# Kernel optimization log

Hardware: AMD Instinct MI355X
Metric: run time of the kernel (lower is better)

## Reference

```python
import jax, jax.numpy as jnp
import numpy as np

B, C, O, N, T, K = 4, 64, 64, 32768, 4, 9
PAD, DIL = 4, 1  # padding*dilation, dilation
SIGMA = 0.05
EPS_BN = 1e-5


def _gather_ch(x, idx):
    # x: [B, C, N], idx: [B, N] -> gather along last dim per channel
    idx3 = jnp.broadcast_to(idx[:, None, :], x.shape)
    return jnp.take_along_axis(x, idx3, axis=-1)


def _weighted_conv(x, coords, w):
    # x: [B,C,N], coords: [B,3,N], w: [O,C,K]
    xp = jnp.pad(x, ((0, 0), (0, 0), (PAD, PAD)))
    cp = jnp.pad(coords, ((0, 0), (0, 0), (PAD, PAD)))
    win_idx = jnp.arange(N)[:, None] + jnp.arange(K) * DIL  # [N, K]
    win = xp[:, :, win_idx]   # [B,C,N,K]
    cwin = cp[:, :, win_idx]  # [B,3,N,K]
    d = cwin - cwin[:, :, :, K // 2:K // 2 + 1]
    s = jnp.sum(d * d, axis=1)                    # [B,N,K]
    r = jnp.sqrt(jnp.where(s > 0, s, 1.0))
    r = jnp.where(s > 0, r, 0.0)
    wgt = jnp.maximum(1.0 - r / SIGMA, 0.0)       # [B,N,K]
    return jnp.einsum('bcnk,bnk,ock->bon', win, wgt, w)


def _bn(x, g, b):
    # training-mode BatchNorm1d over (B, N)
    m = jnp.mean(x, axis=(0, 2), keepdims=True)
    v = jnp.var(x, axis=(0, 2), keepdims=True)
    return g[None, :, None] * (x - m) * jax.lax.rsqrt(v + EPS_BN) + b[None, :, None]


def setup_inputs() -> dict:
    key = jax.random.key(0)
    ks = jax.random.split(key, 12)
    inp = jax.random.normal(ks[0], (B, C, N), dtype=jnp.float32)
    # coords in a small box so sigma=0.05 yields non-trivial weights
    multi_coords = jax.random.uniform(ks[1], (B, 3, N, T), dtype=jnp.float32) * 0.02
    indices = jax.random.randint(ks[2], (B, N, T), 0, N, dtype=jnp.int32)
    reindices = jax.random.randint(ks[3], (B, N, T), 0, N, dtype=jnp.int32)
    fan = C * K
    conv_w = jax.random.normal(ks[4], (T, O, C, K), dtype=jnp.float32) / np.sqrt(fan)
    bn_gamma = jnp.ones((T, O), dtype=jnp.float32)
    bn_beta = jnp.zeros((T, O), dtype=jnp.float32)
    fusion_w = jax.random.normal(ks[5], (O, T * O), dtype=jnp.float32) / np.sqrt(T * O)
    fusion_b = jnp.zeros((O,), dtype=jnp.float32)
    fusion_gamma = jnp.ones((O,), dtype=jnp.float32)
    fusion_beta = jnp.zeros((O,), dtype=jnp.float32)
    return {"input": inp, "multi_coords": multi_coords, "indices": indices,
            "reindices": reindices, "conv_w": conv_w, "bn_gamma": bn_gamma,
            "bn_beta": bn_beta, "fusion_w": fusion_w, "fusion_b": fusion_b,
            "fusion_gamma": fusion_gamma, "fusion_beta": fusion_beta}


def reference(input, multi_coords, indices, reindices, conv_w, bn_gamma, bn_beta,
              fusion_w, fusion_b, fusion_gamma, fusion_beta):
    outs = []
    for i in range(T):  # fixed small set of 4 Hilbert orders
        x = _gather_ch(input, indices[:, :, i])            # [B,C,N]
        x = _weighted_conv(x, multi_coords[:, :, :, i], conv_w[i])  # [B,O,N]
        x = _bn(x, bn_gamma[i], bn_beta[i])
        x = _gather_ch(x, reindices[:, :, i])
        outs.append(x)
    cat = jnp.concatenate(outs, axis=1)                    # [B, T*O, N]
    y = jnp.einsum('bcn,oc->bon', cat, fusion_w) + fusion_b[None, :, None]
    y = _bn(y, fusion_gamma, fusion_beta)
    return jax.nn.relu(y)
```

## Files before the change

kernel.cpp:

```cpp
#include <hip/hip_runtime.h>
#include <hip/hip_bf16.h>

#define BB 4
#define CC 64
#define OO 64
#define NN 32768
#define TT 4
#define KK 9
#define PADW 4
#define SIGMA 0.05f
#define EPS_BN 1e-5f

typedef __attribute__((ext_vector_type(8))) short bf16x8;
typedef __attribute__((ext_vector_type(4))) float f32x4;

__device__ __forceinline__ unsigned short f2bf(float f) {
  __hip_bfloat16 h = __float2bfloat16(f);
  return *reinterpret_cast<unsigned short*>(&h);
}
__device__ __forceinline__ unsigned int pkbf(float a, float b) {
  float2 t; t.x = a; t.y = b;
  __hip_bfloat162 h = __float22bfloat162_rn(t);
  unsigned int r;
  __builtin_memcpy(&r, &h, 4);
  return r;
}

__global__ __launch_bounds__(256) void transpose_kernel(
    const float* __restrict__ inp, unsigned short* __restrict__ xTb)
{
  const int n0 = blockIdx.x * 64;
  const int b  = blockIdx.y;
  const int tid = threadIdx.x;
  __shared__ float xt[64][65];
  {
    int nl = tid & 63, c4 = tid >> 6;
    #pragma unroll
    for (int i = 0; i < 16; ++i) {
      int c = c4 * 16 + i;
      xt[c][nl] = inp[((size_t)(b*CC + c))*NN + n0 + nl];
    }
  }
  __syncthreads();
  {
    int nl = tid >> 2, cq = tid & 3;
    unsigned int pk[8];
    #pragma unroll
    for (int i = 0; i < 8; ++i) {
      int c = cq*16 + i*2;
      pk[i] = pkbf(xt[c][nl], xt[c+1][nl]);
    }
    unsigned int* dst = (unsigned int*)(xTb + (((size_t)b*NN) + n0 + nl)*CC + cq*16);
    ((int4*)dst)[0] = make_int4((int)pk[0],(int)pk[1],(int)pk[2],(int)pk[3]);
    ((int4*)dst)[1] = make_int4((int)pk[4],(int)pk[5],(int)pk[6],(int)pk[7]);
  }
}

__global__ __launch_bounds__(256) void wprep_kernel(
    const float* __restrict__ cw, unsigned short* __restrict__ W4)
{
  const int k = blockIdx.x;
  const int t = blockIdx.y;
  for (int u = threadIdx.x; u < OO*CC; u += 256) {
    int o = u >> 6, c = u & 63;
    int ow = o >> 5, ot = (o >> 4) & 1, l15 = o & 15;
    int frag = c >> 5, q = (c >> 3) & 3, j = c & 7;
    float wv = cw[(((size_t)(t*OO + o))*CC + c)*KK + k];
    W4[(size_t)(t*9+k)*4096 + ow*2048 + ot*1024 + frag*512 + l15*32 + q*8 + j]
        = f2bf(wv);
  }
}

__global__ __launch_bounds__(256, 3) void conv_kernel(
    const unsigned short* __restrict__ xTb,
    const float* __restrict__ mc,
    const int*   __restrict__ ind,
    const unsigned short* __restrict__ W4,
    unsigned short* __restrict__ Y,
    float* __restrict__ cpart2)
{
  const int n0  = blockIdx.x * 256;
  const int b   = blockIdx.y;
  const int t   = blockIdx.z;
  const int tid = threadIdx.x;
  const int lane = tid & 63;
  const int w    = tid >> 6;
  const int l15  = lane & 15;
  const int q    = lane >> 4;
  const int ow   = w & 1;
  const int nw   = w >> 1;

  __shared__ short xg[264*64];
  __shared__ float wgl[256][10];
  __shared__ float mcs[3][268];

  int idxr[9];
  #pragma unroll
  for (int i = 0; i < 9; ++i) {
    int u = tid + 256*i;
    int p = u >> 3;
    int m = n0 + p - PADW;
    idxr[i] = -1;
    if (u < 2112 && m >= 0 && m < NN)
      idxr[i] = ind[((size_t)b*NN + m)*TT + t];
  }

  int4 g[9];
  #pragma unroll
  for (int i = 0; i < 9; ++i) {
    int s = (tid + 256*i) & 7;
    g[i] = make_int4(0,0,0,0);
    if (idxr[i] >= 0)
      g[i] = *(const int4*)(xTb + ((size_t)b*NN + idxr[i])*CC + s*8);
  }

  for (int u = tid; u < 264; u += 256) {
    int m = n0 + u - PADW;
    #pragma unroll
    for (int d = 0; d < 3; ++d) {
      float4 v = make_float4(0.f, 0.f, 0.f, 0.f);
      if (m >= 0 && m < NN)
        v = *(const float4*)(mc + (((size_t)(b*3+d))*NN + m)*TT);
      mcs[d][u] = (t==0) ? v.x : (t==1) ? v.y : (t==2) ? v.z : v.w;
    }
  }

  #pragma unroll
  for (int i = 0; i < 9; ++i) {
    int u = tid + 256*i;
    if (u < 2112) {
      int p = u >> 3, s = u & 7;
      *(int4*)&xg[(p << 6) + ((s ^ (p & 7)) << 3)] = g[i];
    }
  }
  __syncthreads();

  {
    int nl = tid;
    float cx = mcs[0][nl+4], cy = mcs[1][nl+4], cz = mcs[2][nl+4];
    #pragma unroll
    for (int k = 0; k < KK; ++k) {
      float dx = mcs[0][nl+k]-cx, dy = mcs[1][nl+k]-cy, dz = mcs[2][nl+k]-cz;
      float s2 = dx*dx + dy*dy + dz*dz;
      float r = (s2 > 0.f) ? sqrtf(s2) : 0.f;
      wgl[nl][k] = fmaxf(1.f - r*(1.f/SIGMA), 0.f);
    }
  }
  __syncthreads();

  const unsigned short* Wt = W4 + (size_t)t*9*4096 + ow*2048 + (l15*4 + q)*8;
  const f32x4 Z = {0.f, 0.f, 0.f, 0.f};
  f32x4 fin[2][8];
  #pragma unroll
  for (int ot = 0; ot < 2; ++ot)
    #pragma unroll
    for (int ns = 0; ns < 8; ++ns) fin[ot][ns] = Z;

  for (int k = 0; k < KK; ++k) {
    const unsigned short* Wk = Wt + (size_t)k*4096;
    bf16x8 af[2][2];
    #pragma unroll
    for (int ot = 0; ot < 2; ++ot) {
      af[ot][0] = *(const bf16x8*)(Wk + ot*1024);
      af[ot][1] = *(const bf16x8*)(Wk + ot*1024 + 512);
    }
    #pragma unroll
    for (int ns = 0; ns < 8; ++ns) {
      int nl = nw*128 + ns*16 + l15;
      int p  = nl + k;
      const short* row = &xg[p << 6];
      int sw = p & 7;
      bf16x8 b0 = *(const bf16x8*)(row + ((q ^ sw) << 3));
      bf16x8 b1 = *(const bf16x8*)(row + (((4 + q) ^ sw) << 3));
      float wgt = wgl[nl][k];
      #pragma unroll
      for (int ot = 0; ot < 2; ++ot) {
        f32x4 d = __builtin_amdgcn_mfma_f32_16x16x32_bf16(af[ot][0], b0, Z, 0, 0, 0);
        d = __builtin_amdgcn_mfma_f32_16x16x32_bf16(af[ot][1], b1, d, 0, 0, 0);
        fin[ot][ns] += wgt * d;
      }
    }
  }

  #pragma unroll
  for (int ns = 0; ns < 8; ++ns) {
    int nl = nw*128 + ns*16 + l15;
    size_t row = (((size_t)t*BB + b)*NN + n0 + nl)*OO;
    #pragma unroll
    for (int ot = 0; ot < 2; ++ot) {
      uint2 pk2;
      pk2.x = pkbf(fin[ot][ns][0], fin[ot][ns][1]);
      pk2.y = pkbf(fin[ot][ns][2], fin[ot][ns][3]);
      *(uint2*)(Y + row + ow*32 + ot*16 + q*4) = pk2;
    }
  }

  float sv[16];
  #pragma unroll
  for (int ot = 0; ot < 2; ++ot)
    #pragma unroll
    for (int r = 0; r < 4; ++r) {
      float a = 0.f, qs = 0.f;
      #pragma unroll
      for (int ns = 0; ns < 8; ++ns) {
        float v = fin[ot][ns][r];
        a += v; qs += v*v;
      }
      sv[ot*4+r] = a; sv[8+ot*4+r] = qs;
    }
  #pragma unroll
  for (int msk = 1; msk < 16; msk <<= 1) {
    #pragma unroll
    for (int i = 0; i < 16; ++i) sv[i] += __shfl_xor(sv[i], msk, 16);
  }
  if (l15 == 0) {
    int slot4 = ((b*128 + (int)blockIdx.x) << 2) | w;
    #pragma unroll
    for (int ot = 0; ot < 2; ++ot)
      #pragma unroll
      for (int r = 0; r < 4; ++r) {
        int o = ow*32 + ot*16 + q*4 + r;
        cpart2[((size_t)((t*64 + o)*2 + 0))*4096 + slot4] = sv[ot*4+r];
        cpart2[((size_t)((t*64 + o)*2 + 1))*4096 + slot4] = sv[8+ot*4+r];
      }
  }
}

__global__ __launch_bounds__(256) void bnparam_kernel(
    const float* __restrict__ cpart2,
    const float* __restrict__ gam,
    const float* __restrict__ bet,
    float* __restrict__ ss)
{
  const int to = blockIdx.x;
  const int tid = threadIdx.x;
  __shared__ float r1[256], r2[256];
  const float* p1 = cpart2 + (size_t)to*2*4096;
  const float* p2 = p1 + 4096;
  float s1 = 0.f, s2 = 0.f;
  for (int i = tid*4; i < 2048; i += 1024) {
    float4 a = *(const float4*)(p1 + i);
    float4 c = *(const float4*)(p2 + i);
    s1 += a.x + a.y + a.z + a.w;
    s2 += c.x + c.y + c.z + c.w;
  }
  r1[tid] = s1; r2[tid] = s2;
  __syncthreads();
  for (int st = 128; st > 0; st >>= 1) {
    if (tid < st) { r1[tid] += r1[tid+st]; r2[tid] += r2[tid+st]; }
    __syncthreads();
  }
  if (tid == 0) {
    const float inv = 1.f / (float)(BB * NN);
    float mean = r1[0] * inv;
    float var  = r2[0] * inv - mean * mean;
    float sc = gam[to] * rsqrtf(var + EPS_BN);
    ss[to*2 + 0] = sc;
    ss[to*2 + 1] = bet[to] - mean * sc;
  }
}

__global__ __launch_bounds__(256) void wfuse_kernel(
    const float* __restrict__ fw,
    const float* __restrict__ fb,
    const float* __restrict__ ss,
    float* __restrict__ fbp,
    unsigned short* __restrict__ FWB)
{
  const int tid = threadIdx.x;
  {
    int o = tid >> 2, c0 = (tid & 3) * 64;
    float s = 0.f;
    for (int c = c0; c < c0 + 64; ++c)
      s += fw[o*256 + c] * ss[c*2 + 1];
    s += __shfl_xor(s, 1);
    s += __shfl_xor(s, 2);
    if ((tid & 3) == 0) fbp[o] = fb[o] + s;
  }
  for (int e = tid; e < 16384; e += 256) {
    int rk  = e >> 11;
    int ow  = (e >> 10) & 1;
    int ot  = (e >> 9) & 1;
    int l15 = (e >> 5) & 15;
    int cj  = e & 31;
    int o = ow*32 + ot*16 + l15;
    int c = (rk >> 1)*64 + (rk & 1)*32 + cj;
    FWB[e] = f2bf(fw[o*256 + c] * ss[c*2]);
  }
}

__global__ __launch_bounds__(256, 4) void fusion_kernel(
    const unsigned short* __restrict__ Y,
    const int*   __restrict__ rind,
    const unsigned short* __restrict__ FWB,
    const float* __restrict__ fbp,
    float* __restrict__ out,
    float* __restrict__ fpart2)
{
  const int n0  = blockIdx.x * 128;
  const int b   = blockIdx.y;
  const int tid = threadIdx.x;
  const int lane = tid & 63;
  const int w    = tid >> 6;
  const int l15  = lane & 15;
  const int q    = lane >> 4;
  const int ow   = w & 1;
  const int nw   = w >> 1;

  __shared__ short zg[128*64];

  int4 rg[4];
  #pragma unroll
  for (int i = 0; i < 4; ++i) {
    int n = (tid >> 3) + 32*i;
    rg[i] = *(const int4*)(rind + ((size_t)b*NN + n0 + n)*TT);
  }

  f32x4 fin[2][4];
  #pragma unroll
  for (int ot = 0; ot < 2; ++ot)
    #pragma unroll
    for (int ns = 0; ns < 4; ++ns) fin[ot][ns] = (f32x4){0.f,0.f,0.f,0.f};

  #pragma unroll
  for (int r = 0; r < 4; ++r) {
    if (r) __syncthreads();
    #pragma unroll
    for (int i = 0; i < 4; ++i) {
      int u = tid + 256*i;
      int n = u >> 3, s = u & 7;
      int rn = (r == 0) ? rg[i].x : (r == 1) ? rg[i].y
             : (r == 2) ? rg[i].z : rg[i].w;
      int4 raw = *(const int4*)(Y + (((size_t)r*BB + b)*NN + rn)*OO + s*8);
      *(int4*)&zg[(n << 6) + ((s ^ (n & 7)) << 3)] = raw;
    }
    __syncthreads();

    #pragma unroll
    for (int kk = 0; kk < 2; ++kk) {
      int rk = r*2 + kk;
      const unsigned short* wp = FWB + rk*2048 + ow*1024 + (l15*4 + q)*8;
      bf16x8 af[2];
      af[0] = *(const bf16x8*)(wp);
      af[1] = *(const bf16x8*)(wp + 512);
      #pragma unroll
      for (int ns = 0; ns < 4; ++ns) {
        int nl = nw*64 + ns*16 + l15;
        int ch = (kk*4 + q) ^ (nl & 7);
        bf16x8 bfr = *(const bf16x8*)&zg[(nl << 6) + (ch << 3)];
        #pragma unroll
        for (int ot = 0; ot < 2; ++ot)
          fin[ot][ns] = __builtin_amdgcn_mfma_f32_16x16x32_bf16(af[ot], bfr, fin[ot][ns], 0, 0, 0);
      }
    }
  }

  float sv[16];
  #pragma unroll
  for (int ot = 0; ot < 2; ++ot)
    #pragma unroll
    for (int r2 = 0; r2 < 4; ++r2) {
      int o = ow*32 + ot*16 + q*4 + r2;
      float bias = fbp[o];
      float* dst = out + ((size_t)(b*OO + o))*NN + n0 + nw*64;
      float a = 0.f, qs = 0.f;
      #pragma unroll
      for (int ns = 0; ns < 4; ++ns) {
        float v = fin[ot][ns][r2] + bias;
        dst[ns*16 + l15] = v;
        a += v; qs += v*v;
      }
      sv[ot*4+r2] = a; sv[8+ot*4+r2] = qs;
    }
  #pragma unroll
  for (int msk = 1; msk < 16; msk <<= 1) {
    #pragma unroll
    for (int i = 0; i < 16; ++i) sv[i] += __shfl_xor(sv[i], msk, 16);
  }
  if (l15 == 0) {
    int slot4 = ((b*256 + (int)blockIdx.x) << 2) | w;
    #pragma unroll
    for (int ot = 0; ot < 2; ++ot)
      #pragma unroll
      for (int r2 = 0; r2 < 4; ++r2) {
        int o = ow*32 + ot*16 + q*4 + r2;
        fpart2[((size_t)(o*2 + 0))*4096 + slot4] = sv[ot*4+r2];
        fpart2[((size_t)(o*2 + 1))*4096 + slot4] = sv[8+ot*4+r2];
      }
  }
}

__global__ __launch_bounds__(256) void freduce_kernel(
    const float* __restrict__ fpart2,
    const float* __restrict__ fg,
    const float* __restrict__ fbeta,
    float* __restrict__ fss)
{
  const int o = blockIdx.x;
  const int tid = threadIdx.x;
  __shared__ float r1[256], r2[256];
  const float* p1 = fpart2 + (size_t)o*2*4096;
  const float* p2 = p1 + 4096;
  float s1 = 0.f, s2 = 0.f;
  for (int i = tid*4; i < 4096; i += 1024) {
    float4 a = *(const float4*)(p1 + i);
    float4 c = *(const float4*)(p2 + i);
    s1 += a.x + a.y + a.z + a.w;
    s2 += c.x + c.y + c.z + c.w;
  }
  r1[tid] = s1; r2[tid] = s2;
  __syncthreads();
  for (int st = 128; st > 0; st >>= 1) {
    if (tid < st) { r1[tid] += r1[tid+st]; r2[tid] += r2[tid+st]; }
    __syncthreads();
  }
  if (tid == 0) {
    const float inv = 1.f / (float)(BB * NN);
    float mean = r1[0] * inv;
    float var  = r2[0] * inv - mean * mean;
    float sc = fg[o] * rsqrtf(var + EPS_BN);
    fss[o*2 + 0] = sc;
    fss[o*2 + 1] = fbeta[o] - mean * sc;
  }
}

__global__ __launch_bounds__(256) void final_kernel(
    float* __restrict__ out, const float* __restrict__ fss)
{
  const int e0 = blockIdx.x * 2048 + threadIdx.x;
  #pragma unroll
  for (int s = 0; s < 8; ++s) {
    int e  = e0 + s * 256;
    int o2 = (e >> 15) & 63;
    float sc = fss[o2*2 + 0];
    float sh = fss[o2*2 + 1];
    float v = out[e] * sc + sh;
    out[e] = fmaxf(v, 0.f);
  }
}

extern "C" void kernel_launch(void* const* d_in, const int* in_sizes, int n_in,
                              void* d_out, int out_size, void* d_ws, size_t ws_size,
                              hipStream_t stream) {
  const float* inp  = (const float*)d_in[0];
  const float* mc   = (const float*)d_in[1];
  const int*   ind  = (const int*)  d_in[2];
  const int*   rind = (const int*)  d_in[3];
  const float* cw   = (const float*)d_in[4];
  const float* bg   = (const float*)d_in[5];
  const float* bb   = (const float*)d_in[6];
  const float* fw   = (const float*)d_in[7];
  const float* fb   = (const float*)d_in[8];
  const float* fg   = (const float*)d_in[9];
  const float* fbt  = (const float*)d_in[10];

  char* ws = (char*)d_ws;
  float* convss = (float*)(ws + 0);
  float* fss    = (float*)(ws + 2048);
  float* fbp    = (float*)(ws + 3072);
  unsigned short* Y = (unsigned short*)(ws + 8192);
  float* fpart2 = (float*)(ws + 8192 + 67108864);
  unsigned short* FWB = (unsigned short*)(ws + 8192 + 67108864 + 2097152);

  char* ob = (char*)d_out;
  unsigned short* xTb = (unsigned short*)ob;
  unsigned short* W4  = (unsigned short*)(ob + 16777216);
  float*          cpart2 = (float*)(ob + 17072128);
  float* out = (float*)d_out;

  dim3 gt(NN/64, BB);
  transpose_kernel<<<gt, 256, 0, stream>>>(inp, xTb);

  dim3 gw(KK, TT);
  wprep_kernel<<<gw, 256, 0, stream>>>(cw, W4);

  dim3 gc(NN/256, BB, TT);
  conv_kernel<<<gc, 256, 0, stream>>>(xTb, mc, ind, W4, Y, cpart2);

  bnparam_kernel<<<256, 256, 0, stream>>>(cpart2, bg, bb, convss);

  wfuse_kernel<<<1, 256, 0, stream>>>(fw, fb, convss, fbp, FWB);

  dim3 gf(NN/128, BB);
  fusion_kernel<<<gf, 256, 0, stream>>>(Y, rind, FWB, fbp, out, fpart2);

  freduce_kernel<<<OO, 256, 0, stream>>>(fpart2, fg, fbt, fss);

  final_kernel<<<(BB*OO*NN)/2048, 256, 0, stream>>>(out, fss);
}
```

Measured before the change: 223.7 us.

## Pre-transpose indices and coords per order; stage indices in LDS for conv gather

Adds a small kernel that transposes the per-order gather indices and coordinates into contiguous [T,B,N] arrays, so the conv kernel reads them with coalesced strided-free loads instead of picking one lane out of each int4/float4. The conv kernel now stages indices in shared memory and computes geometric weights before the gathered tile is written, overlapping that math with the gather. It also compacts the cpart2 stride to 2048 and raises fusion kernel occupancy hint to 6 blocks. The cost is an extra launch and extra global traffic for the transposed copies, plus an added barrier.

```diff
diff --git a/kernel.cpp b/kernel.cpp
--- a/kernel.cpp
+++ b/kernel.cpp
@@ -71,10 +71,31 @@
   }
 }
 
+__global__ __launch_bounds__(256) void indmc_kernel(
+    const int* __restrict__ ind, const float* __restrict__ mc,
+    int* __restrict__ indT, float* __restrict__ mcT)
+{
+  const int n = blockIdx.x * 256 + threadIdx.x;
+  const int b = blockIdx.y;
+  int4 iv = *(const int4*)(ind + ((size_t)b*NN + n)*TT);
+  indT[((size_t)(0*BB + b))*NN + n] = iv.x;
+  indT[((size_t)(1*BB + b))*NN + n] = iv.y;
+  indT[((size_t)(2*BB + b))*NN + n] = iv.z;
+  indT[((size_t)(3*BB + b))*NN + n] = iv.w;
+  #pragma unroll
+  for (int d = 0; d < 3; ++d) {
+    float4 mv = *(const float4*)(mc + (((size_t)(b*3 + d))*NN + n)*TT);
+    mcT[((size_t)((0*BB + b)*3 + d))*NN + n] = mv.x;
+    mcT[((size_t)((1*BB + b)*3 + d))*NN + n] = mv.y;
+    mcT[((size_t)((2*BB + b)*3 + d))*NN + n] = mv.z;
+    mcT[((size_t)((3*BB + b)*3 + d))*NN + n] = mv.w;
+  }
+}
+
 __global__ __launch_bounds__(256, 3) void conv_kernel(
     const unsigned short* __restrict__ xTb,
-    const float* __restrict__ mc,
-    const int*   __restrict__ ind,
+    const float* __restrict__ mcT,
+    const int*   __restrict__ indT,
     const unsigned short* __restrict__ W4,
     unsigned short* __restrict__ Y,
     float* __restrict__ cpart2)
@@ -93,35 +114,40 @@
   __shared__ short xg[264*64];
   __shared__ float wgl[256][10];
   __shared__ float mcs[3][268];
-
-  int idxr[9];
+  __shared__ int   ids[268];
+
+  for (int u = tid; u < 264; u += 256) {
+    int m = n0 + u - PADW;
+    bool v = (m >= 0) && (m < NN);
+    ids[u] = v ? indT[((size_t)(t*BB + b))*NN + m] : -1;
+    #pragma unroll
+    for (int d = 0; d < 3; ++d)
+      mcs[d][u] = v ? mcT[((size_t)((t*BB + b)*3 + d))*NN + m] : 0.f;
+  }
+  __syncthreads();
+
+  int4 g[9];
   #pragma unroll
   for (int i = 0; i < 9; ++i) {
     int u = tid + 256*i;
-    int p = u >> 3;
-    int m = n0 + p - PADW;
-    idxr[i] = -1;
-    if (u < 2112 && m >= 0 && m < NN)
-      idxr[i] = ind[((size_t)b*NN + m)*TT + t];
-  }
-
-  int4 g[9];
-  #pragma unroll
-  for (int i = 0; i < 9; ++i) {
-    int s = (tid + 256*i) & 7;
     g[i] = make_int4(0,0,0,0);
-    if (idxr[i] >= 0)
-      g[i] = *(const int4*)(xTb + ((size_t)b*NN + idxr[i])*CC + s*8);
-  }
-
-  for (int u = tid; u < 264; u += 256) {
-    int m = n0 + u - PADW;
-    #pragma unroll
-    for (int d = 0; d < 3; ++d) {
-      float4 v = make_float4(0.f, 0.f, 0.f, 0.f);
-      if (m >= 0 && m < NN)
-        v = *(const float4*)(mc + (((size_t)(b*3+d))*NN + m)*TT);
-      mcs[d][u] = (t==0) ? v.x : (t==1) ? v.y : (t==2) ? v.z : v.w;
+    if (u < 2112) {
+      int p = u >> 3, s = u & 7;
+      int idx = ids[p];
+      if (idx >= 0)
+        g[i] = *(const int4*)(xTb + ((size_t)b*NN + idx)*CC + s*8);
+    }
+  }
+
+  {
+    int nl = tid;
+    float cx = mcs[0][nl+4], cy = mcs[1][nl+4], cz = mcs[2][nl+4];
+    #pragma unroll
+    for (int k = 0; k < KK; ++k) {
+      float dx = mcs[0][nl+k]-cx, dy = mcs[1][nl+k]-cy, dz = mcs[2][nl+k]-cz;
+      float s2 = dx*dx + dy*dy + dz*dz;
+      float r = (s2 > 0.f) ? sqrtf(s2) : 0.f;
+      wgl[nl][k] = fmaxf(1.f - r*(1.f/SIGMA), 0.f);
     }
   }
 
@@ -131,19 +157,6 @@
     if (u < 2112) {
       int p = u >> 3, s = u & 7;
       *(int4*)&xg[(p << 6) + ((s ^ (p & 7)) << 3)] = g[i];
-    }
-  }
-  __syncthreads();
-
-  {
-    int nl = tid;
-    float cx = mcs[0][nl+4], cy = mcs[1][nl+4], cz = mcs[2][nl+4];
-    #pragma unroll
-    for (int k = 0; k < KK; ++k) {
-      float dx = mcs[0][nl+k]-cx, dy = mcs[1][nl+k]-cy, dz = mcs[2][nl+k]-cz;
-      float s2 = dx*dx + dy*dy + dz*dz;
-      float r = (s2 > 0.f) ? sqrtf(s2) : 0.f;
-      wgl[nl][k] = fmaxf(1.f - r*(1.f/SIGMA), 0.f);
     }
   }
   __syncthreads();
@@ -220,8 +233,8 @@
       #pragma unroll
       for (int r = 0; r < 4; ++r) {
         int o = ow*32 + ot*16 + q*4 + r;
-        cpart2[((size_t)((t*64 + o)*2 + 0))*4096 + slot4] = sv[ot*4+r];
-        cpart2[((size_t)((t*64 + o)*2 + 1))*4096 + slot4] = sv[8+ot*4+r];
+        cpart2[((size_t)((t*64 + o)*2 + 0))*2048 + slot4] = sv[ot*4+r];
+        cpart2[((size_t)((t*64 + o)*2 + 1))*2048 + slot4] = sv[8+ot*4+r];
       }
   }
 }
@@ -235,8 +248,8 @@
   const int to = blockIdx.x;
   const int tid = threadIdx.x;
   __shared__ float r1[256], r2[256];
-  const float* p1 = cpart2 + (size_t)to*2*4096;
-  const float* p2 = p1 + 4096;
+  const float* p1 = cpart2 + (size_t)to*2*2048;
+  const float* p2 = p1 + 2048;
   float s1 = 0.f, s2 = 0.f;
   for (int i = tid*4; i < 2048; i += 1024) {
     float4 a = *(const float4*)(p1 + i);
@@ -289,7 +302,7 @@
   }
 }
 
-__global__ __launch_bounds__(256, 4) void fusion_kernel(
+__global__ __launch_bounds__(256, 6) void fusion_kernel(
     const unsigned short* __restrict__ Y,
     const int*   __restrict__ rind,
     const unsigned short* __restrict__ FWB,
@@ -465,7 +478,9 @@
   char* ob = (char*)d_out;
   unsigned short* xTb = (unsigned short*)ob;
   unsigned short* W4  = (unsigned short*)(ob + 16777216);
-  float*          cpart2 = (float*)(ob + 17072128);
+  float* cpart2 = (float*)(ob + 17072128);
+  int*   indT   = (int*)  (ob + 21266432);
+  float* mcT    = (float*)(ob + 23363584);
   float* out = (float*)d_out;
 
   dim3 gt(NN/64, BB);
@@ -474,8 +489,11 @@
   dim3 gw(KK, TT);
   wprep_kernel<<<gw, 256, 0, stream>>>(cw, W4);
 
+  dim3 gi(NN/256, BB);
+  indmc_kernel<<<gi, 256, 0, stream>>>(ind, mc, indT, mcT);
+
   dim3 gc(NN/256, BB, TT);
-  conv_kernel<<<gc, 256, 0, stream>>>(xTb, mc, ind, W4, Y, cpart2);
+  conv_kernel<<<gc, 256, 0, stream>>>(xTb, mcT, indT, W4, Y, cpart2);
 
   bnparam_kernel<<<256, 256, 0, stream>>>(cpart2, bg, bb, convss);
 
```

New measurement: 224.6 us. Within noise of the previous version (+0.4%).
